# Performance work log

Hardware: AMD Instinct MI355X
Metric: run time of the kernel (lower is better)

## Reference

```python
import jax, jax.numpy as jnp
import numpy as np

IN, EMB, RNN, OUT = 2, 64, 128, 2
SEQ, PEDS, PRED = 20, 16384, 30


def setup_inputs() -> dict:
    key = jax.random.key(0)
    ks = jax.random.split(key, 6)
    def w(k, shape, fan_in):
        bound = 1.0 / np.sqrt(fan_in)
        return jax.random.uniform(k, shape, jnp.float32, -bound, bound)
    return {
        "observed_batch": jax.random.normal(ks[0], (SEQ, PEDS, IN), jnp.float32),
        "W_emb": w(ks[1], (EMB, IN), IN),
        "b_emb": jnp.zeros((EMB,), jnp.float32),
        "W_ih": w(ks[2], (4 * RNN, EMB), RNN),
        "b_ih": jnp.zeros((4 * RNN,), jnp.float32),
        "W_hh": w(ks[3], (4 * RNN, RNN), RNN),
        "b_hh": jnp.zeros((4 * RNN,), jnp.float32),
        "W_out": w(ks[4], (OUT, RNN), RNN),
        "b_out": jnp.zeros((OUT,), jnp.float32),
        "pred_len": PRED,
    }


def _lstm_cell(x, h, c, W_ih, b_ih, W_hh, b_hh):
    # torch.nn.LSTMCell gate order: i, f, g, o
    gates = x @ W_ih.T + b_ih + h @ W_hh.T + b_hh  # [peds, 4*RNN]
    i, f, g, o = jnp.split(gates, 4, axis=-1)
    i = jax.nn.sigmoid(i)
    f = jax.nn.sigmoid(f)
    g = jnp.tanh(g)
    o = jax.nn.sigmoid(o)
    c_new = f * c + i * g
    h_new = o * jnp.tanh(c_new)
    return h_new, c_new


def reference(observed_batch, W_emb, b_emb, W_ih, b_ih, W_hh, b_hh, W_out, b_out, pred_len):
    peds = observed_batch.shape[1]
    h0 = jnp.zeros((peds, RNN), observed_batch.dtype)
    c0 = jnp.zeros((peds, RNN), observed_batch.dtype)

    # Encode observed steps (dropout is identity in eval mode).
    def enc_step(carry, x_t):
        h, c = carry
        e = jax.nn.relu(x_t @ W_emb.T + b_emb)
        h, c = _lstm_cell(e, h, c, W_ih, b_ih, W_hh, b_hh)
        return (h, c), None

    (h, c), _ = jax.lax.scan(enc_step, (h0, c0), observed_batch)
    # Only the last step's output_layer result is consumed (faithful to source).
    out = h @ W_out.T + b_out  # [peds, OUT]

    def dec_step(carry, _):
        h, c, out = carry
        e = jax.nn.relu(out @ W_emb.T + b_emb)
        h, c = _lstm_cell(e, h, c, W_ih, b_ih, W_hh, b_hh)
        out = h @ W_out.T + b_out
        return (h, c, out), out

    _, output_seq = jax.lax.scan(dec_step, (h, c, out), None, length=pred_len)
    return jnp.squeeze(output_seq)  # [pred_len, peds, 2] (squeeze is a no-op here)
```

## Files before the change

kernel.cpp:

```cpp
#include <hip/hip_runtime.h>
#include <hip/hip_bf16.h>

#define SEQ   20
#define PRED  30
#define TSTEPS (SEQ + PRED)
#define PEDS  16384
#define EMB   64
#define RNN   128
#define PB    64
#define NT    512
#define L2E   1.44269504f

typedef _Float16 half8 __attribute__((ext_vector_type(8)));
typedef __attribute__((ext_vector_type(4))) float f32x4;

__device__ __forceinline__ float sigm2(float xp) {
    return __builtin_amdgcn_rcpf(1.f + __builtin_amdgcn_exp2f(-xp));
}
__device__ __forceinline__ float tanh2p(float xp) {
    float r = __builtin_amdgcn_rcpf(__builtin_amdgcn_exp2f(xp + xp) + 1.f);
    return fmaf(-2.f, r, 1.f);
}
__device__ __forceinline__ float tanh2u(float x) {
    float r = __builtin_amdgcn_rcpf(__builtin_amdgcn_exp2f(x * (2.f * L2E)) + 1.f);
    return fmaf(-2.f, r, 1.f);
}

__global__ void prep_kernel(const float* __restrict__ Wih, const float* __restrict__ Whh,
                            const float* __restrict__ Wemb, const float* __restrict__ bemb,
                            _Float16* __restrict__ Bp, float* __restrict__ ewp) {
    int t = blockIdx.x * blockDim.x + threadIdx.x;
    if (t < 64) {
        ewp[t * 4 + 0] = Wemb[t * 2 + 0];
        ewp[t * 4 + 1] = Wemb[t * 2 + 1];
        ewp[t * 4 + 2] = bemb[t];
        ewp[t * 4 + 3] = 0.f;
    }
    if (t >= 6 * 32 * 64 * 8) return;
    int i  = t & 7;
    int l  = (t >> 3) & 63;
    int nt = (t >> 9) & 31;
    int kt = t >> 14;
    int n = (nt >> 3) * RNN + (nt & 7) * 16 + (l & 15);
    int k = kt * 32 + ((l >> 4) << 3) + i;
    float val = (k < EMB) ? Wih[n * EMB + k] : Whh[n * RNN + (k - EMB)];
    Bp[t] = (_Float16)(val * L2E);
}

__global__ __launch_bounds__(NT, 2) void lstm_kernel(
    const float* __restrict__ obs,
    const float* __restrict__ ewp,
    const float* __restrict__ bih,  const float* __restrict__ bhh,
    const _Float16* __restrict__ Bp,
    const float* __restrict__ Wout, const float* __restrict__ bout,
    float* __restrict__ out)
{
    __shared__ __align__(16) char smA[2 * 24576];
    __shared__ __align__(16) char smB[2 * 32768];
    __shared__ float smEW[64 * 4];
    __shared__ float part[64 * 2 * 4];
    __shared__ float outs[64 * 2];

    const int tid = threadIdx.x;
    const int l   = tid & 63;
    const int w   = __builtin_amdgcn_readfirstlane(tid >> 6);
    const int pg  = blockIdx.x * PB + l;

    for (int r = tid; r < (2 * 24576) / 4; r += NT) ((int*)smA)[r] = 0;
    if (tid < 64) *(f32x4*)(smEW + tid * 4) = *(const f32x4*)(ewp + tid * 4);

    const int jlane = w * 16 + (l & 15);
    const int lrow  = (l >> 4) << 2;
    const int swz   = (l & 7) << 4;

    float bias[4];
#pragma unroll
    for (int g = 0; g < 4; ++g) {
        int n = g * RNN + jlane;
        bias[g] = (bih[n] + bhh[n]) * L2E;
    }

    int aBase[4];
#pragma unroll
    for (int mt = 0; mt < 4; ++mt) {
        int ped = mt * 16 + (l & 15);
        aBase[mt] = ped * 384 + ((l >> 4) << 4);
    }
    int sAddr[4];
#pragma unroll
    for (int r = 0; r < 4; ++r) {
        int ped = lrow + r;
        sAddr[r] = (ped * 384 + 128 + jlane * 2) ^ ((ped & 7) << 4);
    }
    const int eAddr = (l * 384 + w * 16) ^ swz;
    const int oBase = l * 384 + 128 + (w >> 1) * 64;
    const char* bb  = smB + l * 16;
    const char* stageSrc = (const char*)Bp + l * 16 + w * 1024;

    auto stage = [&](int kt, int buf) {
#pragma unroll
        for (int g = 0; g < 4; ++g) {
            const void* src = stageSrc + kt * 32768 + g * 8192;
            __builtin_amdgcn_global_load_lds(
                (const __attribute__((address_space(1))) void*)src,
                (__attribute__((address_space(3))) void*)(smB + buf * 32768 + (g * 8 + w) * 1024),
                16, 0, 0);
        }
    };

    float c[16];
#pragma unroll
    for (int q = 0; q < 16; ++q) c[q] = 0.f;

    stage(0, 0);
    __syncthreads();

    const float* xptr = obs + (size_t)pg * 2;
    int curOff = 0;

    for (int step = 0; step < TSTEPS; ++step) {
        const int nxtOff = curOff ^ 24576;

        {
            float x0, x1;
            if (step < SEQ) {
                x0 = xptr[0]; x1 = xptr[1];
                xptr += PEDS * 2;
            } else {
                x0 = outs[l * 2 + 0];
                x1 = outs[l * 2 + 1];
            }
            half8 vh;
#pragma unroll
            for (int q = 0; q < 8; ++q) {
                const f32x4 ew = *(const f32x4*)(smEW + (w * 8 + q) * 4);
                float v = fmaf(x0, ew[0], fmaf(x1, ew[1], ew[2]));
                vh[q] = (_Float16)fmaxf(v, 0.f);
            }
            *(half8*)(smA + curOff + eAddr) = vh;
        }
        __syncthreads();

        f32x4 acc[4][4];
#pragma unroll
        for (int mt = 0; mt < 4; ++mt)
#pragma unroll
            for (int g = 0; g < 4; ++g) {
                acc[mt][g][0] = bias[g]; acc[mt][g][1] = bias[g];
                acc[mt][g][2] = bias[g]; acc[mt][g][3] = bias[g];
            }
#pragma unroll
        for (int kt = 0; kt < 6; ++kt) {
            const int buf = kt & 1;
            const int ktn = (kt < 5) ? kt + 1 : 0;
            stage(ktn, buf ^ 1);
            asm volatile("s_waitcnt vmcnt(4)" ::: "memory");
            half8 bf[4];
#pragma unroll
            for (int g = 0; g < 4; ++g)
                bf[g] = *(const half8*)(bb + buf * 32768 + (g * 8 + w) * 1024);
#pragma unroll
            for (int mt = 0; mt < 4; ++mt) {
                half8 ah = *(const half8*)(smA + curOff + ((aBase[mt] + kt * 64) ^ swz));
#pragma unroll
                for (int g = 0; g < 4; ++g)
                    acc[mt][g] = __builtin_amdgcn_mfma_f32_16x16x32_f16(ah, bf[g], acc[mt][g], 0, 0, 0);
            }
        }

#pragma unroll
        for (int mt = 0; mt < 4; ++mt) {
#pragma unroll
            for (int r = 0; r < 4; ++r) {
                float gi = acc[mt][0][r], gf = acc[mt][1][r];
                float gg = acc[mt][2][r], go = acc[mt][3][r];
                float i_ = sigm2(gi), f_ = sigm2(gf), g_ = tanh2p(gg), o_ = sigm2(go);
                float cn = fmaf(f_, c[mt * 4 + r], i_ * g_);
                c[mt * 4 + r] = cn;
                float hn = o_ * tanh2u(cn);
                *(_Float16*)(smA + nxtOff + sAddr[r] + mt * 6144) = (_Float16)hn;
            }
        }

        if (step >= SEQ - 1) {
            __syncthreads();
            {
                const int oo = w & 1;
                float s = 0.f;
#pragma unroll
                for (int t = 0; t < 4; ++t) {
                    half8 hh8 = *(const half8*)(smA + nxtOff + ((oBase + t * 16) ^ swz));
                    const f32x4 w0 = *(const f32x4*)(Wout + oo * RNN + (w >> 1) * 32 + t * 8);
                    const f32x4 w1 = *(const f32x4*)(Wout + oo * RNN + (w >> 1) * 32 + t * 8 + 4);
#pragma unroll
                    for (int i = 0; i < 4; ++i) {
                        s = fmaf((float)hh8[i], w0[i], s);
                        s = fmaf((float)hh8[i + 4], w1[i], s);
                    }
                }
                part[(l * 2 + oo) * 4 + (w >> 1)] = s;
            }
            __syncthreads();
            if (tid < 128) {
                int pp = tid & 63, o2 = tid >> 6;
                const float* pr = &part[(pp * 2 + o2) * 4];
                float o = bout[o2] + ((pr[0] + pr[1]) + (pr[2] + pr[3]));
                outs[pp * 2 + o2] = o;
                if (step >= SEQ)
                    out[((size_t)(step - SEQ) * PEDS + (blockIdx.x * PB + pp)) * 2 + o2] = o;
            }
            __syncthreads();
        }
        curOff = nxtOff;
    }
}

extern "C" void kernel_launch(void* const* d_in, const int* in_sizes, int n_in,
                              void* d_out, int out_size, void* d_ws, size_t ws_size,
                              hipStream_t stream) {
    const float* obs  = (const float*)d_in[0];
    const float* Wemb = (const float*)d_in[1];
    const float* bemb = (const float*)d_in[2];
    const float* Wih  = (const float*)d_in[3];
    const float* bih  = (const float*)d_in[4];
    const float* Whh  = (const float*)d_in[5];
    const float* bhh  = (const float*)d_in[6];
    const float* Wout = (const float*)d_in[7];
    const float* bout = (const float*)d_in[8];

    _Float16* Bp  = (_Float16*)d_ws;
    float*    ewp = (float*)(Bp + 6 * 32 * 64 * 8);

    prep_kernel<<<(6 * 32 * 64 * 8 + 255) / 256, 256, 0, stream>>>(Wih, Whh, Wemb, bemb, Bp, ewp);
    lstm_kernel<<<PEDS / PB, NT, 0, stream>>>(obs, ewp, bih, bhh, Bp, Wout, bout, (float*)d_out);
}
```

Measured before the change: 228.7 us.

## Reduce output-projection barriers with wave-shuffle reduction and prefetch observed inputs

Remaps the W_out projection so each group of four lanes computes one (ped, output) dot product and reduces it with shuffles. This removes the partial-sum shared buffer and one block barrier per decode step. W_out is cached in LDS, and the next step's observation is loaded one step ahead to hide global latency. Full __syncthreads are replaced by raw s_barrier sequences that wait only on lgkmcnt, which depends on the outstanding global loads not needing to be visible across waves.

```diff
diff --git a/kernel.cpp b/kernel.cpp
--- a/kernel.cpp
+++ b/kernel.cpp
@@ -13,6 +13,14 @@
 
 typedef _Float16 half8 __attribute__((ext_vector_type(8)));
 typedef __attribute__((ext_vector_type(4))) float f32x4;
+typedef __attribute__((ext_vector_type(2))) float f32x2;
+
+#define RAW_BAR() do {                                          \
+    asm volatile("s_waitcnt lgkmcnt(0)" ::: "memory");          \
+    __builtin_amdgcn_s_barrier();                               \
+    asm volatile("" ::: "memory");                              \
+    __builtin_amdgcn_sched_barrier(0);                          \
+} while (0)
 
 __device__ __forceinline__ float sigm2(float xp) {
     return __builtin_amdgcn_rcpf(1.f + __builtin_amdgcn_exp2f(-xp));
@@ -58,7 +66,7 @@
     __shared__ __align__(16) char smA[2 * 24576];
     __shared__ __align__(16) char smB[2 * 32768];
     __shared__ float smEW[64 * 4];
-    __shared__ float part[64 * 2 * 4];
+    __shared__ float smWO[256];
     __shared__ float outs[64 * 2];
 
     const int tid = threadIdx.x;
@@ -68,6 +76,7 @@
 
     for (int r = tid; r < (2 * 24576) / 4; r += NT) ((int*)smA)[r] = 0;
     if (tid < 64) *(f32x4*)(smEW + tid * 4) = *(const f32x4*)(ewp + tid * 4);
+    if (tid < 256) smWO[tid] = Wout[tid];
 
     const int jlane = w * 16 + (l & 15);
     const int lrow  = (l >> 4) << 2;
@@ -93,9 +102,18 @@
         sAddr[r] = (ped * 384 + 128 + jlane * 2) ^ ((ped & 7) << 4);
     }
     const int eAddr = (l * 384 + w * 16) ^ swz;
-    const int oBase = l * 384 + 128 + (w >> 1) * 64;
     const char* bb  = smB + l * 16;
     const char* stageSrc = (const char*)Bp + l * 16 + w * 1024;
+
+    const int oid  = l >> 2, oq = l & 3;
+    const int oped = (w << 3) + (oid >> 1);
+    const int oo   = oid & 1;
+    const float boutv = bout[oo];
+    int oOff[4];
+#pragma unroll
+    for (int t = 0; t < 4; ++t)
+        oOff[t] = (oped * 384 + 128 + (oq * 32 + t * 8) * 2) ^ ((oped & 7) << 4);
+    const float* woBase = smWO + oo * 128 + oq * 32;
 
     auto stage = [&](int kt, int buf) {
 #pragma unroll
@@ -116,6 +134,8 @@
     __syncthreads();
 
     const float* xptr = obs + (size_t)pg * 2;
+    f32x2 xv = *(const f32x2*)xptr;
+    xptr += PEDS * 2;
     int curOff = 0;
 
     for (int step = 0; step < TSTEPS; ++step) {
@@ -123,13 +143,8 @@
 
         {
             float x0, x1;
-            if (step < SEQ) {
-                x0 = xptr[0]; x1 = xptr[1];
-                xptr += PEDS * 2;
-            } else {
-                x0 = outs[l * 2 + 0];
-                x1 = outs[l * 2 + 1];
-            }
+            if (step < SEQ) { x0 = xv[0]; x1 = xv[1]; }
+            else            { x0 = outs[l * 2 + 0]; x1 = outs[l * 2 + 1]; }
             half8 vh;
 #pragma unroll
             for (int q = 0; q < 8; ++q) {
@@ -139,7 +154,11 @@
             }
             *(half8*)(smA + curOff + eAddr) = vh;
         }
-        __syncthreads();
+        if (step + 1 < SEQ) {
+            xv = *(const f32x2*)xptr;
+            xptr += PEDS * 2;
+        }
+        RAW_BAR();
 
         f32x4 acc[4][4];
 #pragma unroll
@@ -183,33 +202,28 @@
         }
 
         if (step >= SEQ - 1) {
-            __syncthreads();
-            {
-                const int oo = w & 1;
-                float s = 0.f;
-#pragma unroll
-                for (int t = 0; t < 4; ++t) {
-                    half8 hh8 = *(const half8*)(smA + nxtOff + ((oBase + t * 16) ^ swz));
-                    const f32x4 w0 = *(const f32x4*)(Wout + oo * RNN + (w >> 1) * 32 + t * 8);
-                    const f32x4 w1 = *(const f32x4*)(Wout + oo * RNN + (w >> 1) * 32 + t * 8 + 4);
-#pragma unroll
-                    for (int i = 0; i < 4; ++i) {
-                        s = fmaf((float)hh8[i], w0[i], s);
-                        s = fmaf((float)hh8[i + 4], w1[i], s);
-                    }
+            RAW_BAR();
+            float s = 0.f;
+#pragma unroll
+            for (int t = 0; t < 4; ++t) {
+                half8 hh8 = *(const half8*)(smA + nxtOff + oOff[t]);
+                const f32x4 w0 = *(const f32x4*)(woBase + t * 8);
+                const f32x4 w1 = *(const f32x4*)(woBase + t * 8 + 4);
+#pragma unroll
+                for (int i = 0; i < 4; ++i) {
+                    s = fmaf((float)hh8[i], w0[i], s);
+                    s = fmaf((float)hh8[i + 4], w1[i], s);
                 }
-                part[(l * 2 + oo) * 4 + (w >> 1)] = s;
-            }
-            __syncthreads();
-            if (tid < 128) {
-                int pp = tid & 63, o2 = tid >> 6;
-                const float* pr = &part[(pp * 2 + o2) * 4];
-                float o = bout[o2] + ((pr[0] + pr[1]) + (pr[2] + pr[3]));
-                outs[pp * 2 + o2] = o;
+            }
+            s += __shfl_xor(s, 1);
+            s += __shfl_xor(s, 2);
+            if (oq == 0) {
+                float ov = s + boutv;
+                outs[oped * 2 + oo] = ov;
                 if (step >= SEQ)
-                    out[((size_t)(step - SEQ) * PEDS + (blockIdx.x * PB + pp)) * 2 + o2] = o;
-            }
-            __syncthreads();
+                    out[((size_t)(step - SEQ) * PEDS + blockIdx.x * PB + oped) * 2 + oo] = ov;
+            }
+            RAW_BAR();
         }
         curOff = nxtOff;
     }
```

After: 234.9 us. 2.7% more time.

## Triple-buffer weight staging, stage inputs in LDS, use barriers without vmcnt waits

Applied to the files above, without the earlier changes.

The per-wave weight-slice staging through global_load_lds goes from double to triple buffering, prefetching two k-slices ahead with a matching vmcnt(8) wait. The __syncthreads calls become a raw s_barrier that only waits on lgkmcnt, so in-flight prefetches are not drained at every barrier. Observed inputs and W_out are copied into LDS up front, removing per-step global loads. LDS use grows close to the per-CU limit, and correctness now depends on each wave reading only the weight regions it staged itself.

```diff
diff --git a/kernel.cpp b/kernel.cpp
--- a/kernel.cpp
+++ b/kernel.cpp
@@ -13,6 +13,14 @@
 
 typedef _Float16 half8 __attribute__((ext_vector_type(8)));
 typedef __attribute__((ext_vector_type(4))) float f32x4;
+typedef __attribute__((ext_vector_type(2))) float f32x2;
+
+#define RAW_BAR() do {                                          \
+    asm volatile("s_waitcnt lgkmcnt(0)" ::: "memory");          \
+    __builtin_amdgcn_s_barrier();                               \
+    asm volatile("" ::: "memory");                              \
+    __builtin_amdgcn_sched_barrier(0);                          \
+} while (0)
 
 __device__ __forceinline__ float sigm2(float xp) {
     return __builtin_amdgcn_rcpf(1.f + __builtin_amdgcn_exp2f(-xp));
@@ -56,18 +64,24 @@
     float* __restrict__ out)
 {
     __shared__ __align__(16) char smA[2 * 24576];
-    __shared__ __align__(16) char smB[2 * 32768];
+    __shared__ __align__(16) char smB[3 * 32768];
+    __shared__ float smObs[SEQ * 128];
     __shared__ float smEW[64 * 4];
+    __shared__ float smWO[256];
     __shared__ float part[64 * 2 * 4];
     __shared__ float outs[64 * 2];
 
     const int tid = threadIdx.x;
     const int l   = tid & 63;
     const int w   = __builtin_amdgcn_readfirstlane(tid >> 6);
-    const int pg  = blockIdx.x * PB + l;
 
     for (int r = tid; r < (2 * 24576) / 4; r += NT) ((int*)smA)[r] = 0;
     if (tid < 64) *(f32x4*)(smEW + tid * 4) = *(const f32x4*)(ewp + tid * 4);
+    if (tid < 256) smWO[tid] = Wout[tid];
+    for (int i = tid; i < SEQ * 128; i += NT) {
+        int st = i >> 7, r = i & 127;
+        smObs[i] = obs[(size_t)st * (PEDS * 2) + blockIdx.x * 128 + r];
+    }
 
     const int jlane = w * 16 + (l & 15);
     const int lrow  = (l >> 4) << 2;
@@ -96,11 +110,13 @@
     const int oBase = l * 384 + 128 + (w >> 1) * 64;
     const char* bb  = smB + l * 16;
     const char* stageSrc = (const char*)Bp + l * 16 + w * 1024;
-
-    auto stage = [&](int kt, int buf) {
+    const float* woBase = smWO + (w & 1) * 128 + (w >> 1) * 32;
+
+    auto stage = [&](int slice) {
+        const int buf = slice % 3;
 #pragma unroll
         for (int g = 0; g < 4; ++g) {
-            const void* src = stageSrc + kt * 32768 + g * 8192;
+            const void* src = stageSrc + slice * 32768 + g * 8192;
             __builtin_amdgcn_global_load_lds(
                 (const __attribute__((address_space(1))) void*)src,
                 (__attribute__((address_space(3))) void*)(smB + buf * 32768 + (g * 8 + w) * 1024),
@@ -112,10 +128,10 @@
 #pragma unroll
     for (int q = 0; q < 16; ++q) c[q] = 0.f;
 
-    stage(0, 0);
+    stage(0);
+    stage(1);
     __syncthreads();
 
-    const float* xptr = obs + (size_t)pg * 2;
     int curOff = 0;
 
     for (int step = 0; step < TSTEPS; ++step) {
@@ -124,8 +140,8 @@
         {
             float x0, x1;
             if (step < SEQ) {
-                x0 = xptr[0]; x1 = xptr[1];
-                xptr += PEDS * 2;
+                f32x2 xv = *(const f32x2*)(smObs + step * 128 + l * 2);
+                x0 = xv[0]; x1 = xv[1];
             } else {
                 x0 = outs[l * 2 + 0];
                 x1 = outs[l * 2 + 1];
@@ -139,7 +155,7 @@
             }
             *(half8*)(smA + curOff + eAddr) = vh;
         }
-        __syncthreads();
+        RAW_BAR();
 
         f32x4 acc[4][4];
 #pragma unroll
@@ -151,10 +167,9 @@
             }
 #pragma unroll
         for (int kt = 0; kt < 6; ++kt) {
-            const int buf = kt & 1;
-            const int ktn = (kt < 5) ? kt + 1 : 0;
-            stage(ktn, buf ^ 1);
-            asm volatile("s_waitcnt vmcnt(4)" ::: "memory");
+            const int buf = kt % 3;
+            stage((kt < 4) ? kt + 2 : kt - 4);
+            asm volatile("s_waitcnt vmcnt(8)" ::: "memory");
             half8 bf[4];
 #pragma unroll
             for (int g = 0; g < 4; ++g)
@@ -183,15 +198,15 @@
         }
 
         if (step >= SEQ - 1) {
-            __syncthreads();
+            RAW_BAR();
             {
                 const int oo = w & 1;
                 float s = 0.f;
 #pragma unroll
                 for (int t = 0; t < 4; ++t) {
                     half8 hh8 = *(const half8*)(smA + nxtOff + ((oBase + t * 16) ^ swz));
-                    const f32x4 w0 = *(const f32x4*)(Wout + oo * RNN + (w >> 1) * 32 + t * 8);
-                    const f32x4 w1 = *(const f32x4*)(Wout + oo * RNN + (w >> 1) * 32 + t * 8 + 4);
+                    const f32x4 w0 = *(const f32x4*)(woBase + t * 8);
+                    const f32x4 w1 = *(const f32x4*)(woBase + t * 8 + 4);
 #pragma unroll
                     for (int i = 0; i < 4; ++i) {
                         s = fmaf((float)hh8[i], w0[i], s);
@@ -200,16 +215,16 @@
                 }
                 part[(l * 2 + oo) * 4 + (w >> 1)] = s;
             }
-            __syncthreads();
+            RAW_BAR();
             if (tid < 128) {
                 int pp = tid & 63, o2 = tid >> 6;
                 const float* pr = &part[(pp * 2 + o2) * 4];
                 float o = bout[o2] + ((pr[0] + pr[1]) + (pr[2] + pr[3]));
                 outs[pp * 2 + o2] = o;
                 if (step >= SEQ)
-                    out[((size_t)(step - SEQ) * PEDS + (blockIdx.x * PB + pp)) * 2 + o2] = o;
-            }
-            __syncthreads();
+                    out[((size_t)(step - SEQ) * PEDS + blockIdx.x * PB + pp) * 2 + o2] = o;
+            }
+            RAW_BAR();
         }
         curOff = nxtOff;
     }
```

Measured after the change: 228.1 us, median of 2. No clear change (-0.3%).
